# Kernel optimization log

Hardware: AMD Instinct MI355X
Metric: run time of the kernel (lower is better)

## Reference

```python
import jax, jax.numpy as jnp
import numpy as np

BLK = 46  # hardcoded block size in the original module
EPS = 1e-5


def setup_inputs() -> dict:
    key = jax.random.key(0)
    ks = jax.random.split(key, 13)
    N, C, Ci = 128, 512, 256
    return {
        "ori_feature": jax.random.normal(ks[0], (N, C, BLK), jnp.float32),
        "bn_gamma": jax.random.uniform(ks[1], (C,), jnp.float32),
        "bn_beta": jax.random.normal(ks[2], (C,), jnp.float32),
        "bn_mean": jax.random.normal(ks[3], (C,), jnp.float32),
        "bn_var": jax.random.uniform(ks[4], (C,), jnp.float32),
        "theta_w": jax.random.normal(ks[5], (Ci, C), jnp.float32) * 0.02,
        "theta_b": jax.random.normal(ks[6], (Ci,), jnp.float32) * 0.02,
        "phi_w": jax.random.normal(ks[7], (Ci, C), jnp.float32) * 0.02,
        "phi_b": jax.random.normal(ks[8], (Ci,), jnp.float32) * 0.02,
        "g_w": jax.random.normal(ks[9], (Ci, C), jnp.float32) * 0.02,
        "g_b": jax.random.normal(ks[10], (Ci,), jnp.float32) * 0.02,
        "W_w": jax.random.normal(ks[11], (C, Ci), jnp.float32) * 0.02,
        "W_b": jax.random.normal(ks[12], (C,), jnp.float32) * 0.02,
    }


def reference(ori_feature, bn_gamma, bn_beta, bn_mean, bn_var,
              theta_w, theta_b, phi_w, phi_b, g_w, g_b, W_w, W_b):
    N, C, num = ori_feature.shape  # (N, C, 46)
    # BatchNorm1d (inference-style, per-channel) + ReLU
    inv = bn_gamma / jnp.sqrt(bn_var + EPS)
    feat = jax.nn.relu(ori_feature * inv[None, :, None]
                       + (bn_beta - bn_mean * inv)[None, :, None])
    feat = feat.transpose(0, 2, 1).reshape(N * num, C)  # (T, C)
    x_theta = feat @ theta_w.T + theta_b  # (T, Ci)
    x_phi = feat @ phi_w.T + phi_b        # (T, Ci)
    attn = x_theta @ x_phi.T              # (T, T)
    # block-diagonal masking: entries within the same 46-token block set to -1000
    blk = jnp.arange(N * num) // num
    attn = jnp.where(blk[:, None] == blk[None, :], jnp.float32(-1000.0), attn)
    f_div_C = jax.nn.softmax(attn, axis=-1)
    g_x = feat @ g_w.T + g_b              # (T, Ci)
    y = f_div_C @ g_x                     # (T, Ci)
    W_y = (y @ W_w.T + W_b).reshape(N, num, C)
    att_fea = ori_feature.transpose(0, 2, 1) + W_y  # (N, 46, C)
    return att_fea, f_div_C
```

## Files before the change

kernel.cpp:

```cpp
#include <hip/hip_runtime.h>
#include <math.h>

#define N_BATCH 128
#define C_DIM   512
#define BLKSZ   46
#define T_DIM   (N_BATCH * BLKSZ)
#define CI      256
#define EPS_BN  1e-5f
#define NCB     (T_DIM / 128)

typedef __attribute__((ext_vector_type(8))) short bf16x8;
typedef __attribute__((ext_vector_type(4))) float f32x4;

__device__ __forceinline__ short f2bf(float f) {
    union { float f; unsigned u; } v; v.f = f;
    unsigned r = v.u + 0x7fffu + ((v.u >> 16) & 1u);
    return (short)(r >> 16);
}

__device__ __forceinline__ void gload16(const void* g, void* l) {
    __builtin_amdgcn_global_load_lds((__attribute__((address_space(1))) void*)g,
                                     (__attribute__((address_space(3))) void*)l,
                                     16, 0, 0);
}

__global__ __launch_bounds__(256) void bn_relu_kernel(
    const float* __restrict__ ori, const float* __restrict__ gamma,
    const float* __restrict__ beta, const float* __restrict__ mean,
    const float* __restrict__ var, short* __restrict__ feat)
{
    __shared__ short tile[256 * BLKSZ];
    const int n = blockIdx.y;
    const int c0 = blockIdx.x * 256;
    const int tid = threadIdx.x;
    for (int i = tid; i < 256 * BLKSZ; i += 256) {
        int cl = i / BLKSZ, b = i - cl * BLKSZ;
        int c = c0 + cl;
        float inv = gamma[c] * rsqrtf(var[c] + EPS_BN);
        float v = ori[((size_t)n * C_DIM + c) * BLKSZ + b] * inv + (beta[c] - mean[c] * inv);
        tile[cl * BLKSZ + b] = f2bf(fmaxf(v, 0.0f));
    }
    __syncthreads();
    for (int i = tid; i < BLKSZ * 256; i += 256) {
        int b = i >> 8, cl = i & 255;
        feat[(size_t)(n * BLKSZ + b) * C_DIM + c0 + cl] = tile[cl * BLKSZ + b];
    }
}

__global__ __launch_bounds__(256) void cvt_kernel(
    const float* __restrict__ thw, const float* __restrict__ phw,
    const float* __restrict__ gw, const float* __restrict__ Ww,
    const float* __restrict__ thb, const float* __restrict__ phb,
    short* __restrict__ wcat, short* __restrict__ wg,
    short* __restrict__ wW, float* __restrict__ bcat)
{
    const int i = blockIdx.x * 256 + threadIdx.x;
    const float* src[4] = {thw, phw, gw, Ww};
    short* dst[4] = {wcat, wcat + 256 * 512, wg, wW};
    #pragma unroll
    for (int m = 0; m < 4; ++m) {
        float4 v = *(const float4*)(src[m] + (size_t)i * 4);
        short4 t = make_short4(f2bf(v.x), f2bf(v.y), f2bf(v.z), f2bf(v.w));
        *(short4*)(dst[m] + (size_t)i * 4) = t;
    }
    if (blockIdx.x == 0) {
        bcat[threadIdx.x] = thb[threadIdx.x];
        bcat[threadIdx.x + 256] = phb[threadIdx.x];
    }
}

template <int EPI, bool ACVT, int BM, int BN>
__global__ __launch_bounds__(256, 2) void gemm_nt(
    const void* __restrict__ Avoid, const short* __restrict__ B,
    const float* __restrict__ bias, void* __restrict__ Cvoid,
    int M, int Nn, int K, int lda, int ldb, int nsplit,
    const float* __restrict__ ori,
    float* __restrict__ stats, const float* __restrict__ rowstat,
    float* __restrict__ fout)
{
    constexpr int NWC = BN / 64;
    __shared__ short As[BM * 32];
    __shared__ short Bs[BN * 32];
    const int tid = threadIdx.x;
    const int w = tid >> 6, lane = tid & 63;
    const int m0 = blockIdx.y * BM, n0 = blockIdx.x * BN;
    const int wr = w / NWC, wc = w % NWC;

    const int kper = K / 32 / nsplit;
    const int kt0 = blockIdx.z * kper, kt1 = kt0 + kper;

    f32x4 acc[4][4] = {};

    const int sr = tid >> 2;
    const int sc = (tid & 3) * 8;
    const short* Ab = (const short*)Avoid;
    const float* Af = (const float*)Avoid;

    float rm = 0.f, rz = 0.f;
    int a_r = 0, a_c = 0;
    if constexpr (ACVT) {
        constexpr int EPT = BM / 8;
        constexpr int TPR = 32 / EPT;
        a_r = tid / TPR;
        a_c = (tid % TPR) * EPT;
        float2 st = ((const float2*)rowstat)[m0 + a_r];
        rm = st.x; rz = st.y;
    }

    for (int kt = kt0; kt < kt1; ++kt) {
        const int k0 = kt * 32;
        if constexpr (!ACVT) {
            #pragma unroll
            for (int p = 0; p < BM / 64; ++p)
                gload16(Ab + (size_t)(m0 + p * 64 + sr) * lda + k0 + sc,
                        &As[(p * 64 + sr) * 32 + sc]);
        } else {
            constexpr int EPT = BM / 8;
            const float* src = Af + (size_t)(m0 + a_r) * lda + k0 + a_c;
            float* fd = fout + (size_t)(m0 + a_r) * lda + k0 + a_c;
            short tmp[EPT] __attribute__((aligned(16)));
            #pragma unroll
            for (int q = 0; q < EPT / 4; ++q) {
                float4 v = *(const float4*)(src + q * 4);
                float4 e;
                e.x = expf(v.x - rm) * rz;
                e.y = expf(v.y - rm) * rz;
                e.z = expf(v.z - rm) * rz;
                e.w = expf(v.w - rm) * rz;
                *(float4*)(fd + q * 4) = e;
                tmp[q * 4 + 0] = f2bf(e.x); tmp[q * 4 + 1] = f2bf(e.y);
                tmp[q * 4 + 2] = f2bf(e.z); tmp[q * 4 + 3] = f2bf(e.w);
            }
            #pragma unroll
            for (int q = 0; q < EPT / 8; ++q)
                *(bf16x8*)&As[a_r * 32 + a_c + q * 8] = *(bf16x8*)&tmp[q * 8];
        }
        #pragma unroll
        for (int p = 0; p < BN / 64; ++p)
            gload16(B + (size_t)(n0 + p * 64 + sr) * ldb + k0 + sc,
                    &Bs[(p * 64 + sr) * 32 + sc]);
        __syncthreads();

        bf16x8 af[4], bfr[4];
        #pragma unroll
        for (int i = 0; i < 4; ++i)
            af[i] = *(bf16x8*)&As[(wr * 64 + i * 16 + (lane & 15)) * 32 + (lane >> 4) * 8];
        #pragma unroll
        for (int j = 0; j < 4; ++j)
            bfr[j] = *(bf16x8*)&Bs[(wc * 64 + j * 16 + (lane & 15)) * 32 + (lane >> 4) * 8];
        #pragma unroll
        for (int i = 0; i < 4; ++i)
            #pragma unroll
            for (int j = 0; j < 4; ++j)
                acc[i][j] = __builtin_amdgcn_mfma_f32_16x16x32_bf16(af[i], bfr[j], acc[i][j], 0, 0, 0);
        __syncthreads();
    }

    const int col = lane & 15, rowq = lane >> 4;

    if constexpr (EPI == 5) {
        __shared__ float sm[NWC][BM];
        __shared__ float ss[NWC][BM];
        int cbj[4];
        #pragma unroll
        for (int j = 0; j < 4; ++j)
            cbj[j] = (n0 + wc * 64 + j * 16 + col) / BLKSZ;
        #pragma unroll
        for (int i = 0; i < 4; ++i) {
            #pragma unroll
            for (int r = 0; r < 4; ++r) {
                const int trow = wr * 64 + i * 16 + rowq * 4 + r;
                const int grow = m0 + trow;
                const int rb = grow / BLKSZ;
                float vj[4];
                float vmax = -1e30f;
                #pragma unroll
                for (int j = 0; j < 4; ++j) {
                    float v = acc[i][j][r];
                    if (cbj[j] == rb) v = -30000.0f;
                    vj[j] = v;
                    ((float*)Cvoid)[(size_t)grow * Nn + (n0 + wc * 64 + j * 16 + col)] = v;
                    vmax = fmaxf(vmax, v);
                }
                #pragma unroll
                for (int off = 1; off < 16; off <<= 1)
                    vmax = fmaxf(vmax, __shfl_xor(vmax, off));
                float s = 0.f;
                #pragma unroll
                for (int j = 0; j < 4; ++j) s += expf(vj[j] - vmax);
                #pragma unroll
                for (int off = 1; off < 16; off <<= 1)
                    s += __shfl_xor(s, off);
                if (col == 0) { sm[wc][trow] = vmax; ss[wc][trow] = s; }
            }
        }
        __syncthreads();
        if (tid < BM) {
            const float ma = sm[0][tid], mb = sm[1][tid];
            const float mx = fmaxf(ma, mb);
            const float S = ss[0][tid] * expf(ma - mx) + ss[1][tid] * expf(mb - mx);
            ((float2*)stats)[(size_t)blockIdx.x * M + (m0 + tid)] = make_float2(mx, S);
        }
    } else {
        #pragma unroll
        for (int i = 0; i < 4; ++i) {
            #pragma unroll
            for (int j = 0; j < 4; ++j) {
                #pragma unroll
                for (int r = 0; r < 4; ++r) {
                    const int grow = m0 + wr * 64 + i * 16 + rowq * 4 + r;
                    const int gcol = n0 + wc * 64 + j * 16 + col;
                    const float v = acc[i][j][r];
                    if (EPI == 1) {
                        ((short*)Cvoid)[(size_t)grow * Nn + gcol] = f2bf(v + bias[gcol]);
                    } else if (EPI == 2) {
                        ((short*)Cvoid)[(size_t)grow * Nn + gcol] = f2bf(v + bias[grow]);
                    } else if (EPI == 3) {
                        ((float*)Cvoid)[(size_t)blockIdx.z * M * Nn + (size_t)grow * Nn + gcol] = v;
                    } else {
                        const int nb = grow / BLKSZ, bb = grow - nb * BLKSZ;
                        ((float*)Cvoid)[(size_t)grow * Nn + gcol] =
                            v + bias[gcol] + ori[((size_t)nb * C_DIM + gcol) * BLKSZ + bb];
                    }
                }
            }
        }
    }
}

__global__ __launch_bounds__(256) void combine_stats_kernel(
    const float* __restrict__ stats, float* __restrict__ rowstat)
{
    const int row = blockIdx.x * 256 + threadIdx.x;
    float m = -1e30f, Z = 0.f;
    for (int cb = 0; cb < NCB; ++cb) {
        float2 p = ((const float2*)stats)[(size_t)cb * T_DIM + row];
        float nm = fmaxf(m, p.x);
        Z = Z * expf(m - nm) + p.y * expf(p.x - nm);
        m = nm;
    }
    ((float2*)rowstat)[row] = make_float2(m, 1.0f / Z);
}

__global__ __launch_bounds__(256) void reduce_y_kernel(
    const float* __restrict__ part, short* __restrict__ y, int ns)
{
    const size_t i = (size_t)blockIdx.x * 256 + threadIdx.x;
    float4 s = *(const float4*)(part + i * 4);
    for (int z = 1; z < ns; ++z) {
        float4 v = *(const float4*)(part + (size_t)z * T_DIM * CI + i * 4);
        s.x += v.x; s.y += v.y; s.z += v.z; s.w += v.w;
    }
    short4 t = make_short4(f2bf(s.x), f2bf(s.y), f2bf(s.z), f2bf(s.w));
    *(short4*)(y + i * 4) = t;
}

extern "C" void kernel_launch(void* const* d_in, const int* in_sizes, int n_in,
                              void* d_out, int out_size, void* d_ws, size_t ws_size,
                              hipStream_t stream)
{
    const float* ori     = (const float*)d_in[0];
    const float* gamma   = (const float*)d_in[1];
    const float* beta    = (const float*)d_in[2];
    const float* mean    = (const float*)d_in[3];
    const float* var     = (const float*)d_in[4];
    const float* theta_w = (const float*)d_in[5];
    const float* theta_b = (const float*)d_in[6];
    const float* phi_w   = (const float*)d_in[7];
    const float* phi_b   = (const float*)d_in[8];
    const float* g_w     = (const float*)d_in[9];
    const float* g_b     = (const float*)d_in[10];
    const float* W_w     = (const float*)d_in[11];
    const float* W_b     = (const float*)d_in[12];

    float* out = (float*)d_out;
    float* P   = out + (size_t)T_DIM * C_DIM;

    char* wsb = (char*)d_ws;
    short* feat = (short*)wsb;  wsb += (size_t)T_DIM * C_DIM * 2;
    short* xcat = (short*)wsb;  wsb += (size_t)T_DIM * 512 * 2;
    short* gxT  = (short*)wsb;  wsb += (size_t)CI * T_DIM * 2;
    short* wcat = (short*)wsb;  wsb += (size_t)512 * C_DIM * 2;
    short* wg   = (short*)wsb;  wsb += (size_t)CI * C_DIM * 2;
    short* wW   = (short*)wsb;  wsb += (size_t)C_DIM * CI * 2;
    float* bcat = (float*)wsb;  wsb += 512 * 4;
    short* ybf  = (short*)wsb;  wsb += (size_t)T_DIM * CI * 2;
    float* rowstat = (float*)wsb; wsb += (size_t)T_DIM * 8;
    float* ypart= (float*)wsb;
    float* stats = ypart;

    const size_t base = (size_t)((char*)ypart - (char*)d_ws);
    const int ns = (ws_size >= base + 4u * (size_t)T_DIM * CI * 4u) ? 4 : 2;

    bn_relu_kernel<<<dim3(2, 128), 256, 0, stream>>>(ori, gamma, beta, mean, var, feat);
    cvt_kernel<<<128, 256, 0, stream>>>(theta_w, phi_w, g_w, W_w, theta_b, phi_b,
                                        wcat, wg, wW, bcat);

    gemm_nt<1, false, 128, 128><<<dim3(4, T_DIM / 128), 256, 0, stream>>>(
        feat, wcat, bcat, xcat, T_DIM, 512, C_DIM, C_DIM, C_DIM, 1, nullptr,
        nullptr, nullptr, nullptr);

    gemm_nt<2, false, 128, 128><<<dim3(T_DIM / 128, CI / 128), 256, 0, stream>>>(
        wg, feat, g_b, gxT, CI, T_DIM, C_DIM, C_DIM, C_DIM, 1, nullptr,
        nullptr, nullptr, nullptr);

    gemm_nt<5, false, 128, 128><<<dim3(T_DIM / 128, T_DIM / 128), 256, 0, stream>>>(
        xcat, xcat + CI, nullptr, P, T_DIM, T_DIM, CI, 512, 512, 1, nullptr,
        stats, nullptr, nullptr);

    combine_stats_kernel<<<T_DIM / 256, 256, 0, stream>>>(stats, rowstat);

    gemm_nt<3, true, 64, 256><<<dim3(1, T_DIM / 64, ns), 256, 0, stream>>>(
        P, gxT, nullptr, ypart, T_DIM, CI, T_DIM, T_DIM, T_DIM, ns, nullptr,
        nullptr, rowstat, P);
    reduce_y_kernel<<<(T_DIM * CI / 4) / 256, 256, 0, stream>>>(ypart, ybf, ns);

    gemm_nt<4, false, 128, 128><<<dim3(C_DIM / 128, T_DIM / 128), 256, 0, stream>>>(
        ybf, wW, W_b, out, T_DIM, C_DIM, CI, CI, CI, 1, ori,
        nullptr, nullptr, nullptr);
}
```

Baseline: 358.9 us.

## Store raw attention logits as fp16 scratch and shrink PV GEMM row tile

```diff
diff --git a/kernel.cpp b/kernel.cpp
--- a/kernel.cpp
+++ b/kernel.cpp
@@ -16,6 +16,13 @@
     union { float f; unsigned u; } v; v.f = f;
     unsigned r = v.u + 0x7fffu + ((v.u >> 16) & 1u);
     return (short)(r >> 16);
+}
+
+__device__ __forceinline__ float h2f(unsigned short h) {
+    _Float16 x; __builtin_memcpy(&x, &h, 2); return (float)x;
+}
+__device__ __forceinline__ unsigned short f2h(float f) {
+    _Float16 x = (_Float16)f; unsigned short u; __builtin_memcpy(&u, &x, 2); return u;
 }
 
 __device__ __forceinline__ void gload16(const void* g, void* l) {
@@ -69,7 +76,7 @@
     }
 }
 
-template <int EPI, bool ACVT, int BM, int BN>
+template <int EPI, int ACVT, int BM, int BN>
 __global__ __launch_bounds__(256, 2) void gemm_nt(
     const void* __restrict__ Avoid, const short* __restrict__ B,
     const float* __restrict__ bias, void* __restrict__ Cvoid,
@@ -79,27 +86,32 @@
     float* __restrict__ fout)
 {
     constexpr int NWC = BN / 64;
+    constexpr int NWR = 4 / NWC;
+    constexpr int MI  = BM / (NWR * 16);
+    static_assert((EPI != 5 && EPI != 6) || NWC == 2, "stats epilogue assumes NWC==2");
     __shared__ short As[BM * 32];
     __shared__ short Bs[BN * 32];
     const int tid = threadIdx.x;
     const int w = tid >> 6, lane = tid & 63;
     const int m0 = blockIdx.y * BM, n0 = blockIdx.x * BN;
     const int wr = w / NWC, wc = w % NWC;
+    const int wrow = wr * (MI * 16);
 
     const int kper = K / 32 / nsplit;
     const int kt0 = blockIdx.z * kper, kt1 = kt0 + kper;
 
-    f32x4 acc[4][4] = {};
+    f32x4 acc[MI][4] = {};
 
     const int sr = tid >> 2;
     const int sc = (tid & 3) * 8;
     const short* Ab = (const short*)Avoid;
     const float* Af = (const float*)Avoid;
+    const unsigned short* Ah = (const unsigned short*)Avoid;
 
     float rm = 0.f, rz = 0.f;
     int a_r = 0, a_c = 0;
-    if constexpr (ACVT) {
-        constexpr int EPT = BM / 8;
+    if constexpr (ACVT != 0) {
+        constexpr int EPT = BM * 32 / 256;
         constexpr int TPR = 32 / EPT;
         a_r = tid / TPR;
         a_c = (tid % TPR) * EPT;
@@ -109,31 +121,39 @@
 
     for (int kt = kt0; kt < kt1; ++kt) {
         const int k0 = kt * 32;
-        if constexpr (!ACVT) {
+        if constexpr (ACVT == 0) {
             #pragma unroll
             for (int p = 0; p < BM / 64; ++p)
                 gload16(Ab + (size_t)(m0 + p * 64 + sr) * lda + k0 + sc,
                         &As[(p * 64 + sr) * 32 + sc]);
         } else {
-            constexpr int EPT = BM / 8;
-            const float* src = Af + (size_t)(m0 + a_r) * lda + k0 + a_c;
-            float* fd = fout + (size_t)(m0 + a_r) * lda + k0 + a_c;
+            constexpr int EPT = BM * 32 / 256;
+            const int k0c = k0 + a_c;
+            float* fd = fout + (size_t)(m0 + a_r) * lda + k0c;
             short tmp[EPT] __attribute__((aligned(16)));
             #pragma unroll
             for (int q = 0; q < EPT / 4; ++q) {
-                float4 v = *(const float4*)(src + q * 4);
                 float4 e;
-                e.x = expf(v.x - rm) * rz;
-                e.y = expf(v.y - rm) * rz;
-                e.z = expf(v.z - rm) * rz;
-                e.w = expf(v.w - rm) * rz;
+                if constexpr (ACVT == 1) {
+                    float4 v = *(const float4*)(Af + (size_t)(m0 + a_r) * lda + k0c + q * 4);
+                    e.x = expf(v.x - rm) * rz;
+                    e.y = expf(v.y - rm) * rz;
+                    e.z = expf(v.z - rm) * rz;
+                    e.w = expf(v.w - rm) * rz;
+                } else {
+                    ushort4 hv = *(const ushort4*)(Ah + (size_t)(m0 + a_r) * lda + k0c + q * 4);
+                    e.x = expf(h2f(hv.x) - rm) * rz;
+                    e.y = expf(h2f(hv.y) - rm) * rz;
+                    e.z = expf(h2f(hv.z) - rm) * rz;
+                    e.w = expf(h2f(hv.w) - rm) * rz;
+                }
                 *(float4*)(fd + q * 4) = e;
                 tmp[q * 4 + 0] = f2bf(e.x); tmp[q * 4 + 1] = f2bf(e.y);
                 tmp[q * 4 + 2] = f2bf(e.z); tmp[q * 4 + 3] = f2bf(e.w);
             }
             #pragma unroll
-            for (int q = 0; q < EPT / 8; ++q)
-                *(bf16x8*)&As[a_r * 32 + a_c + q * 8] = *(bf16x8*)&tmp[q * 8];
+            for (int q = 0; q < EPT / 4; ++q)
+                *(short4*)&As[a_r * 32 + a_c + q * 4] = *(short4*)&tmp[q * 4];
         }
         #pragma unroll
         for (int p = 0; p < BN / 64; ++p)
@@ -141,15 +161,15 @@
                     &Bs[(p * 64 + sr) * 32 + sc]);
         __syncthreads();
 
-        bf16x8 af[4], bfr[4];
-        #pragma unroll
-        for (int i = 0; i < 4; ++i)
-            af[i] = *(bf16x8*)&As[(wr * 64 + i * 16 + (lane & 15)) * 32 + (lane >> 4) * 8];
+        bf16x8 af[MI], bfr[4];
+        #pragma unroll
+        for (int i = 0; i < MI; ++i)
+            af[i] = *(bf16x8*)&As[(wrow + i * 16 + (lane & 15)) * 32 + (lane >> 4) * 8];
         #pragma unroll
         for (int j = 0; j < 4; ++j)
             bfr[j] = *(bf16x8*)&Bs[(wc * 64 + j * 16 + (lane & 15)) * 32 + (lane >> 4) * 8];
         #pragma unroll
-        for (int i = 0; i < 4; ++i)
+        for (int i = 0; i < MI; ++i)
             #pragma unroll
             for (int j = 0; j < 4; ++j)
                 acc[i][j] = __builtin_amdgcn_mfma_f32_16x16x32_bf16(af[i], bfr[j], acc[i][j], 0, 0, 0);
@@ -158,7 +178,7 @@
 
     const int col = lane & 15, rowq = lane >> 4;
 
-    if constexpr (EPI == 5) {
+    if constexpr (EPI == 5 || EPI == 6) {
         __shared__ float sm[NWC][BM];
         __shared__ float ss[NWC][BM];
         int cbj[4];
@@ -166,10 +186,10 @@
         for (int j = 0; j < 4; ++j)
             cbj[j] = (n0 + wc * 64 + j * 16 + col) / BLKSZ;
         #pragma unroll
-        for (int i = 0; i < 4; ++i) {
+        for (int i = 0; i < MI; ++i) {
             #pragma unroll
             for (int r = 0; r < 4; ++r) {
-                const int trow = wr * 64 + i * 16 + rowq * 4 + r;
+                const int trow = wrow + i * 16 + rowq * 4 + r;
                 const int grow = m0 + trow;
                 const int rb = grow / BLKSZ;
                 float vj[4];
@@ -178,8 +198,15 @@
                 for (int j = 0; j < 4; ++j) {
                     float v = acc[i][j][r];
                     if (cbj[j] == rb) v = -30000.0f;
+                    const size_t idx = (size_t)grow * Nn + (n0 + wc * 64 + j * 16 + col);
+                    if constexpr (EPI == 6) {
+                        unsigned short hh = f2h(v);
+                        ((unsigned short*)Cvoid)[idx] = hh;
+                        v = h2f(hh);
+                    } else {
+                        ((float*)Cvoid)[idx] = v;
+                    }
                     vj[j] = v;
-                    ((float*)Cvoid)[(size_t)grow * Nn + (n0 + wc * 64 + j * 16 + col)] = v;
                     vmax = fmaxf(vmax, v);
                 }
                 #pragma unroll
@@ -203,12 +230,12 @@
         }
     } else {
         #pragma unroll
-        for (int i = 0; i < 4; ++i) {
+        for (int i = 0; i < MI; ++i) {
             #pragma unroll
             for (int j = 0; j < 4; ++j) {
                 #pragma unroll
                 for (int r = 0; r < 4; ++r) {
-                    const int grow = m0 + wr * 64 + i * 16 + rowq * 4 + r;
+                    const int grow = m0 + wrow + i * 16 + rowq * 4 + r;
                     const int gcol = n0 + wc * 64 + j * 16 + col;
                     const float v = acc[i][j][r];
                     if (EPI == 1) {
@@ -286,36 +313,53 @@
     float* bcat = (float*)wsb;  wsb += 512 * 4;
     short* ybf  = (short*)wsb;  wsb += (size_t)T_DIM * CI * 2;
     float* rowstat = (float*)wsb; wsb += (size_t)T_DIM * 8;
-    float* ypart= (float*)wsb;
-    float* stats = ypart;
-
-    const size_t base = (size_t)((char*)ypart - (char*)d_ws);
-    const int ns = (ws_size >= base + 4u * (size_t)T_DIM * CI * 4u) ? 4 : 2;
+
+    const size_t base   = (size_t)(wsb - (char*)d_ws);
+    const size_t p16sz  = (size_t)T_DIM * T_DIM * 2;
+    const size_t ypsz4  = 4u * (size_t)T_DIM * CI * 4u;
+    const bool bigws = ws_size >= base + p16sz + ypsz4;
 
     bn_relu_kernel<<<dim3(2, 128), 256, 0, stream>>>(ori, gamma, beta, mean, var, feat);
     cvt_kernel<<<128, 256, 0, stream>>>(theta_w, phi_w, g_w, W_w, theta_b, phi_b,
                                         wcat, wg, wW, bcat);
 
-    gemm_nt<1, false, 128, 128><<<dim3(4, T_DIM / 128), 256, 0, stream>>>(
+    gemm_nt<1, 0, 128, 128><<<dim3(4, T_DIM / 128), 256, 0, stream>>>(
         feat, wcat, bcat, xcat, T_DIM, 512, C_DIM, C_DIM, C_DIM, 1, nullptr,
         nullptr, nullptr, nullptr);
 
-    gemm_nt<2, false, 128, 128><<<dim3(T_DIM / 128, CI / 128), 256, 0, stream>>>(
+    gemm_nt<2, 0, 128, 128><<<dim3(T_DIM / 128, CI / 128), 256, 0, stream>>>(
         wg, feat, g_b, gxT, CI, T_DIM, C_DIM, C_DIM, C_DIM, 1, nullptr,
         nullptr, nullptr, nullptr);
 
-    gemm_nt<5, false, 128, 128><<<dim3(T_DIM / 128, T_DIM / 128), 256, 0, stream>>>(
-        xcat, xcat + CI, nullptr, P, T_DIM, T_DIM, CI, 512, 512, 1, nullptr,
-        stats, nullptr, nullptr);
-
-    combine_stats_kernel<<<T_DIM / 256, 256, 0, stream>>>(stats, rowstat);
-
-    gemm_nt<3, true, 64, 256><<<dim3(1, T_DIM / 64, ns), 256, 0, stream>>>(
-        P, gxT, nullptr, ypart, T_DIM, CI, T_DIM, T_DIM, T_DIM, ns, nullptr,
-        nullptr, rowstat, P);
-    reduce_y_kernel<<<(T_DIM * CI / 4) / 256, 256, 0, stream>>>(ypart, ybf, ns);
-
-    gemm_nt<4, false, 128, 128><<<dim3(C_DIM / 128, T_DIM / 128), 256, 0, stream>>>(
+    if (bigws) {
+        unsigned short* p16 = (unsigned short*)wsb;
+        float* ypart = (float*)(wsb + p16sz);
+        float* stats = ypart;
+
+        gemm_nt<6, 0, 128, 128><<<dim3(T_DIM / 128, T_DIM / 128), 256, 0, stream>>>(
+            xcat, xcat + CI, nullptr, p16, T_DIM, T_DIM, CI, 512, 512, 1, nullptr,
+            stats, nullptr, nullptr);
+        combine_stats_kernel<<<T_DIM / 256, 256, 0, stream>>>(stats, rowstat);
+        gemm_nt<3, 2, 32, 256><<<dim3(1, T_DIM / 32, 4), 256, 0, stream>>>(
+            p16, gxT, nullptr, ypart, T_DIM, CI, T_DIM, T_DIM, T_DIM, 4, nullptr,
+            nullptr, rowstat, P);
+        reduce_y_kernel<<<(T_DIM * CI / 4) / 256, 256, 0, stream>>>(ypart, ybf, 4);
+    } else {
+        float* ypart = (float*)wsb;
+        float* stats = ypart;
+        const int ns = (ws_size >= base + ypsz4) ? 4 : 2;
+
+        gemm_nt<5, 0, 128, 128><<<dim3(T_DIM / 128, T_DIM / 128), 256, 0, stream>>>(
+            xcat, xcat + CI, nullptr, P, T_DIM, T_DIM, CI, 512, 512, 1, nullptr,
+            stats, nullptr, nullptr);
+        combine_stats_kernel<<<T_DIM / 256, 256, 0, stream>>>(stats, rowstat);
+        gemm_nt<3, 1, 32, 256><<<dim3(1, T_DIM / 32, ns), 256, 0, stream>>>(
+            P, gxT, nullptr, ypart, T_DIM, CI, T_DIM, T_DIM, T_DIM, ns, nullptr,
+            nullptr, rowstat, P);
+        reduce_y_kernel<<<(T_DIM * CI / 4) / 256, 256, 0, stream>>>(ypart, ybf, ns);
+    }
+
+    gemm_nt<4, 0, 128, 128><<<dim3(C_DIM / 128, T_DIM / 128), 256, 0, stream>>>(
         ybf, wW, W_b, out, T_DIM, C_DIM, CI, CI, CI, 1, ori,
         nullptr, nullptr, nullptr);
 }
```

After: 350.5 us. 1.02x faster.
